# Kernel tuning notes

Hardware: AMD Instinct MI355X
Metric: run time of the kernel (lower is better)

Reference implementation:

```python
import jax, jax.numpy as jnp
import numpy as np

B, S, D, H = 4, 2048, 512, 8
HD = D // H  # head_dim = 64


def setup_inputs() -> dict:
    key = jax.random.key(0)
    ks = jax.random.split(key, 16)
    sd = 1.0 / np.sqrt(D)
    def lin(ka, kb):
        W = jax.random.uniform(ka, (D, D), jnp.float32, -sd, sd)
        b = jax.random.uniform(kb, (D,), jnp.float32, -sd, sd)
        return W, b
    Wq, bq = lin(ks[0], ks[1])
    Wk, bk = lin(ks[2], ks[3])
    Wv, bv = lin(ks[4], ks[5])
    Wo, bo = lin(ks[6], ks[7])
    Ws, bs = lin(ks[8], ks[9])
    Wsh, bsh = lin(ks[10], ks[11])
    mod1_feat = jax.random.normal(ks[12], (B, S, D), jnp.float32)
    mod2_feat = jax.random.normal(ks[13], (B, S, D), jnp.float32)
    return {"mod1_feat": mod1_feat, "mod2_feat": mod2_feat,
            "Wq": Wq, "bq": bq, "Wk": Wk, "bk": bk, "Wv": Wv, "bv": bv,
            "Wo": Wo, "bo": bo, "Ws": Ws, "bs": bs, "Wsh": Wsh, "bsh": bsh}


def _heads(x):
    # [B, S, D] -> [B, H, S, HD]
    b, s, _ = x.shape
    return x.reshape(b, s, H, HD).transpose(0, 2, 1, 3)


def reference(mod1_feat, mod2_feat, Wq, bq, Wk, bk, Wv, bv, Wo, bo, Ws, bs, Wsh, bsh):
    Q = _heads(mod1_feat @ Wq + bq)
    K = _heads(mod2_feat @ Wk + bk)
    V = _heads(mod2_feat @ Wv + bv)
    scale = _heads(mod2_feat @ Ws + bs)
    shift = _heads(mod2_feat @ Wsh + bsh)
    K = K * scale + shift
    V = V * scale + shift
    scores = jnp.einsum('bhqd,bhkd->bhqk', Q, K) / jnp.sqrt(jnp.float32(HD))
    attn = jax.nn.softmax(scores, axis=-1)
    out = jnp.einsum('bhqk,bhkd->bhqd', attn, V)  # [B, H, S, HD]
    out = out.transpose(0, 2, 1, 3).reshape(mod1_feat.shape[0], -1, H * HD)
    return out @ Wo + bo
```

## Files before the change

### kernel.cpp

```cpp
#include <hip/hip_runtime.h>
#include <hip/hip_bf16.h>
#include <cstdint>
#include <cstddef>

typedef __bf16 bf16_t;
typedef __bf16 bf16x8 __attribute__((ext_vector_type(8)));
typedef __bf16 bf16x4 __attribute__((ext_vector_type(4)));
typedef float f32x4 __attribute__((ext_vector_type(4)));

#define DEVINL static __device__ __forceinline__

constexpr int B_ = 4, S_ = 2048, D_ = 512, H_ = 8, HD_ = 64;
constexpr int M_ = B_ * S_;
constexpr int NIN = 14;

DEVINL bf16x8 load8g(const bf16_t* p) { return *reinterpret_cast<const bf16x8*>(p); }

DEVINL int swcol(int col, int row) {
  return (col & ~63) | ((((col >> 3) ^ row) & 7) << 3) | (col & 7);
}

DEVINL int pK(int row) { return (row & 3) | (((row >> 3) & 1) << 2); }
DEVINL int swcolK(int col, int row) {
  return (col & ~63) | ((((col >> 3) ^ pK(row)) & 7) << 3) | (col & 7);
}

DEVINL void gl2lds(const bf16_t* g, bf16_t* l) {
  __builtin_amdgcn_global_load_lds(
      (const __attribute__((address_space(1))) void*)g,
      (__attribute__((address_space(3))) void*)l, 16, 0, 0);
}

DEVINL void stage16(bf16_t* dst, const void* src, size_t off, bool f32) {
  if (f32) {
    const float* p = (const float*)src + off;
    bf16x8 v0, v1;
#pragma unroll
    for (int j = 0; j < 8; ++j) { v0[j] = (bf16_t)p[j]; v1[j] = (bf16_t)p[8 + j]; }
    *reinterpret_cast<bf16x8*>(dst)     = v0;
    *reinterpret_cast<bf16x8*>(dst + 8) = v1;
  } else {
    const bf16_t* p = (const bf16_t*)src + off;
    *reinterpret_cast<bf16x8*>(dst)     = load8g(p);
    *reinterpret_cast<bf16x8*>(dst + 8) = load8g(p + 8);
  }
}

DEVINL float readf(const void* p, size_t i, bool f32) {
  return f32 ? ((const float*)p)[i] : (float)((const bf16_t*)p)[i];
}

struct DetectArgs { const uint16_t* p[NIN]; int n[NIN]; int* flags; };

__global__ __launch_bounds__(64) void detect_kernel(DetectArgs a) {
  const int z = blockIdx.x;
  const uint16_t* p = a.p[z];
  const int n = a.n[z];
  const int t = threadIdx.x;
  int cnt = 0;
  for (int i = t; i < n; i += 64) {
    const int e = (p[i] >> 7) & 0xFF;
    cnt += (e >= 200);
  }
#pragma unroll
  for (int off = 32; off > 0; off >>= 1) cnt += __shfl_down(cnt, off, 64);
  if (t == 0) a.flags[z] = (cnt > 16) ? 1 : 0;
}

struct PrepArgs {
  const void* csrc[2]; bf16_t* cdst[2]; int cidx[2];
  const void* wsrc[6]; int wIdx[6]; bf16_t* wdst[6];
  const int* flags;
};

__global__ __launch_bounds__(256) void prep_kernel(PrepArgs a) {
  __shared__ bf16_t tile[64][80];
  const int bid = blockIdx.x;
  if (bid < 4096) {
    const int z = bid >> 11;
    const int bx = bid & 2047;
    const bool f32 = a.flags[a.cidx[z]] != 0;
    const size_t i = ((size_t)bx * 256 + threadIdx.x) * 8;
    const int row = (int)(i >> 9);
    const int col = (int)(i & 511);
    bf16_t* dst = a.cdst[z] + (size_t)row * 512 + swcol(col, row);
    if (f32) {
      const float* p = (const float*)a.csrc[z] + i;
      bf16x8 v;
#pragma unroll
      for (int j = 0; j < 8; ++j) v[j] = (bf16_t)p[j];
      *reinterpret_cast<bf16x8*>(dst) = v;
    } else {
      *reinterpret_cast<bf16x8*>(dst) = load8g((const bf16_t*)a.csrc[z] + i);
    }
  } else {
    const int rem = bid - 4096;
    const int w = rem >> 6;
    const int r6 = rem & 63;
    const int k0 = (r6 & 7) * 64, n0 = (r6 >> 3) * 64;
    const void* src = a.wsrc[w];
    const bool f32 = a.flags[a.wIdx[w]] != 0;
    bf16_t* dst = a.wdst[w];
    const int t = threadIdx.x;
    const int r = t >> 2, c0 = (t & 3) * 16;
    stage16(&tile[r][c0], src, (size_t)(k0 + r) * 512 + n0 + c0, f32);
    __syncthreads();
    const int orow = n0 + r;
    bf16_t* o = dst + (size_t)orow * 512;
#pragma unroll
    for (int half = 0; half < 2; ++half) {
      bf16x8 ov;
#pragma unroll
      for (int j = 0; j < 8; ++j) ov[j] = tile[c0 + half * 8 + j][r];
      *reinterpret_cast<bf16x8*>(o + swcol(k0 + c0 + half * 8, orow)) = ov;
    }
  }
}

struct GemmBatch {
  const bf16_t* A[3];
  const bf16_t* Bt[3];
  const void* bias[3]; int bIdx[3];
  void* C[3];          int cIdx[3];
  const int* flags;
};

__global__ __launch_bounds__(512) void gemm_bt_kernel(GemmBatch args) {
  constexpr int K = 512, N = 512;
  __shared__ bf16_t As[3][128][64];
  __shared__ bf16_t Bs[3][64][64];
  const int z = blockIdx.z;
  const bf16_t* Ag  = args.A[z];
  const bf16_t* Btg = args.Bt[z];
  const int m0 = blockIdx.x * 128, n0 = blockIdx.y * 64;
  const int t = threadIdx.x, lane = t & 63, wave = t >> 6;
  const int l16 = lane & 15, quad = lane >> 4;
  const int wm = wave * 16;
  const int lr = lane >> 3, lc = (lane & 7) * 8;

  auto stage = [&](int slot, int k0) {
#pragma unroll
    for (int s = 0; s < 2; ++s) {
      const int r = wm + s * 8;
      gl2lds(Ag + (size_t)(m0 + r + lr) * K + k0 + lc, &As[slot][r][0]);
    }
    gl2lds(Btg + (size_t)(n0 + wave * 8 + lr) * K + k0 + lc, &Bs[slot][wave * 8][0]);
  };

  f32x4 acc[4] = {};

  stage(0, 0);
  stage(1, 64);

  constexpr int NT = K / 64;
  int cur = 0;
  for (int kt = 0; kt < NT - 1; ++kt) {
    asm volatile("s_waitcnt vmcnt(3)\n\ts_barrier" ::: "memory");
    __builtin_amdgcn_sched_barrier(0);
    if (kt + 2 < NT) {
      const int slot2 = cur == 0 ? 2 : cur - 1;
      stage(slot2, (kt + 2) * 64);
    }
#pragma unroll
    for (int ks = 0; ks < 2; ++ks) {
      const int sw = swcol(ks * 32 + quad * 8, l16);
      bf16x8 af = *reinterpret_cast<const bf16x8*>(&As[cur][wm + l16][sw]);
      bf16x8 bfr[4];
#pragma unroll
      for (int j = 0; j < 4; ++j)
        bfr[j] = *reinterpret_cast<const bf16x8*>(&Bs[cur][j * 16 + l16][sw]);
#pragma unroll
      for (int j = 0; j < 4; ++j)
        acc[j] = __builtin_amdgcn_mfma_f32_16x16x32_bf16(af, bfr[j], acc[j], 0, 0, 0);
    }
    cur = (cur == 2) ? 0 : cur + 1;
  }
  asm volatile("s_waitcnt vmcnt(0)\n\ts_barrier" ::: "memory");
  __builtin_amdgcn_sched_barrier(0);
#pragma unroll
  for (int ks = 0; ks < 2; ++ks) {
    const int sw = swcol(ks * 32 + quad * 8, l16);
    bf16x8 af = *reinterpret_cast<const bf16x8*>(&As[cur][wm + l16][sw]);
    bf16x8 bfr[4];
#pragma unroll
    for (int j = 0; j < 4; ++j)
      bfr[j] = *reinterpret_cast<const bf16x8*>(&Bs[cur][j * 16 + l16][sw]);
#pragma unroll
    for (int j = 0; j < 4; ++j)
      acc[j] = __builtin_amdgcn_mfma_f32_16x16x32_bf16(af, bfr[j], acc[j], 0, 0, 0);
  }

  const void* biag = args.bias[z];
  void* Cg         = args.C[z];
  const bool bf32 = args.bIdx[z] >= 0 && args.flags[args.bIdx[z]];
  const bool cf32 = args.cIdx[z] >= 0 && args.flags[args.cIdx[z]];
#pragma unroll
  for (int j = 0; j < 4; ++j) {
    const int col = n0 + j * 16 + l16;
    const float bv = readf(biag, col, bf32);
    const int rowb = m0 + wm + quad * 4;
#pragma unroll
    for (int r = 0; r < 4; ++r) {
      const size_t idx = (size_t)(rowb + r) * N + col;
      const float v = acc[j][r] + bv;
      if (cf32) ((float*)Cg)[idx] = v;
      else      ((bf16_t*)Cg)[idx] = (bf16_t)v;
    }
  }
}

struct KsvArgs {
  const bf16_t* A;
  const bf16_t* Bt[4];
  const void* bias[4]; int bIdx[4];
  bf16_t* Kmod;
  bf16_t* VtT;
  const int* flags;
};

__global__ __launch_bounds__(1024) void ksv_kernel(KsvArgs args) {
  constexpr int K = 512;
  __shared__ bf16_t As[3][128][64];
  __shared__ bf16_t Bs[3][4][64][64];
  const int m0 = blockIdx.x * 128, n0 = blockIdx.y * 64;
  const int t = threadIdx.x, lane = t & 63, wave = t >> 6;
  const int l16 = lane & 15, quad = lane >> 4;
  const int wm = (wave >> 2) * 32;
  const int wn = (wave & 3) * 16;
  const int lr = lane >> 3, lc = (lane & 7) * 8;

  auto stage = [&](int slot, int k0) {
    gl2lds(args.A + (size_t)(m0 + wave * 8 + lr) * K + k0 + lc, &As[slot][wave * 8][0]);
    const int mat = wave >> 2;
    const int rb = (wave & 3) * 16;
#pragma unroll
    for (int s = 0; s < 2; ++s) {
      const int r = rb + s * 8;
      gl2lds(args.Bt[mat] + (size_t)(n0 + r + lr) * K + k0 + lc, &Bs[slot][mat][r][0]);
    }
  };

  f32x4 acc[4][2] = {};

  stage(0, 0);
  stage(1, 64);

  constexpr int NT = K / 64;
  int cur = 0;
  for (int kt = 0; kt < NT - 1; ++kt) {
    asm volatile("s_waitcnt vmcnt(3)\n\ts_barrier" ::: "memory");
    __builtin_amdgcn_sched_barrier(0);
    if (kt + 2 < NT) {
      const int slot2 = cur == 0 ? 2 : cur - 1;
      stage(slot2, (kt + 2) * 64);
    }
#pragma unroll
    for (int ks = 0; ks < 2; ++ks) {
      const int sw = swcol(ks * 32 + quad * 8, l16);
      bf16x8 af[2], bfr[4];
#pragma unroll
      for (int mi = 0; mi < 2; ++mi)
        af[mi] = *reinterpret_cast<const bf16x8*>(&As[cur][wm + mi * 16 + l16][sw]);
#pragma unroll
      for (int mat = 0; mat < 4; ++mat)
        bfr[mat] = *reinterpret_cast<const bf16x8*>(&Bs[cur][mat][wn + l16][sw]);
#pragma unroll
      for (int mat = 0; mat < 4; ++mat)
#pragma unroll
        for (int mi = 0; mi < 2; ++mi)
          acc[mat][mi] = __builtin_amdgcn_mfma_f32_16x16x32_bf16(af[mi], bfr[mat], acc[mat][mi], 0, 0, 0);
    }
    cur = (cur == 2) ? 0 : cur + 1;
  }
  asm volatile("s_waitcnt vmcnt(0)\n\ts_barrier" ::: "memory");
  __builtin_amdgcn_sched_barrier(0);
#pragma unroll
  for (int ks = 0; ks < 2; ++ks) {
    const int sw = swcol(ks * 32 + quad * 8, l16);
    bf16x8 af[2], bfr[4];
#pragma unroll
    for (int mi = 0; mi < 2; ++mi)
      af[mi] = *reinterpret_cast<const bf16x8*>(&As[cur][wm + mi * 16 + l16][sw]);
#pragma unroll
    for (int mat = 0; mat < 4; ++mat)
      bfr[mat] = *reinterpret_cast<const bf16x8*>(&Bs[cur][mat][wn + l16][sw]);
#pragma unroll
    for (int mat = 0; mat < 4; ++mat)
#pragma unroll
      for (int mi = 0; mi < 2; ++mi)
        acc[mat][mi] = __builtin_amdgcn_mfma_f32_16x16x32_bf16(af[mi], bfr[mat], acc[mat][mi], 0, 0, 0);
  }

  const int col = n0 + wn + l16;
  const float bk  = readf(args.bias[0], col, args.bIdx[0] >= 0 && args.flags[args.bIdx[0]]);
  const float bv  = readf(args.bias[1], col, args.bIdx[1] >= 0 && args.flags[args.bIdx[1]]);
  const float bs  = readf(args.bias[2], col, args.bIdx[2] >= 0 && args.flags[args.bIdx[2]]);
  const float bsh = readf(args.bias[3], col, args.bIdx[3] >= 0 && args.flags[args.bIdx[3]]);
  const int hh = col >> 6, dd = col & 63;
#pragma unroll
  for (int mi = 0; mi < 2; ++mi) {
    const int rowb = m0 + wm + mi * 16 + quad * 4;
    bf16x4 vpack;
#pragma unroll
    for (int r = 0; r < 4; ++r) {
      const int row = rowb + r;
      const float s  = acc[2][mi][r] + bs;
      const float sh = acc[3][mi][r] + bsh;
      const float kk = fmaf(acc[0][mi][r] + bk, s, sh);
      const float vv = fmaf(acc[1][mi][r] + bv, s, sh);
      args.Kmod[(size_t)row * 512 + swcolK(col, row)] = (bf16_t)kk;
      vpack[r] = (bf16_t)vv;
    }
    const int bb = rowb >> 11;
    const int ss = rowb & 2047;
    *reinterpret_cast<bf16x4*>(
        args.VtT + (((size_t)(bb * H_ + hh)) * HD_ + dd) * S_ + swcol(ss, dd)) = vpack;
  }
}

__global__ __launch_bounds__(512) void attn_kernel(const bf16_t* Q, const bf16_t* Kb,
                                                   const bf16_t* Vt, bf16_t* O) {
  __shared__ bf16_t Ks[3][64][64];
  __shared__ bf16_t Vs[3][64][64];
  const int i = blockIdx.x;
  const int xcd = i & 7, g = i >> 3;
  const int slice = xcd * 4 + (g & 3);
  const int qt = g >> 2;
  const int b = slice >> 3, h = slice & 7;
  const int t = threadIdx.x, wave = t >> 6, lane = t & 63;
  const int l16 = lane & 15, quad = lane >> 4;
  const int q0 = qt * 128 + wave * 16;
  const int lr = lane >> 3, lc = (lane & 7) * 8;

  bf16x8 ones;
#pragma unroll
  for (int j = 0; j < 8; ++j) ones[j] = (bf16_t)1.0f;

  bf16x8 qf[2];
  {
    const size_t qrow = ((size_t)b * S_ + q0 + l16) * D_ + h * HD_;
    qf[0] = load8g(Q + qrow + quad * 8);
    qf[1] = load8g(Q + qrow + 32 + quad * 8);
  }

  f32x4 oacc[4] = {};
  f32x4 lacc = {};

  const size_t kbase = (size_t)b * S_ * D_ + h * HD_;
  const size_t vbase = ((size_t)(b * H_ + h)) * HD_ * S_;

  const int rbase = ((l16 >> 2) << 3) | (l16 & 3);
  int koff[2][4];
#pragma unroll
  for (int j = 0; j < 4; ++j) {
    const int rho = rbase + (j >> 1) * 32 + (j & 1) * 4;
#pragma unroll
    for (int dc = 0; dc < 2; ++dc)
      koff[dc][j] = rho * 64 + swcolK(dc * 32 + quad * 8, rho);
  }
  const int voff[2] = { swcol(quad * 8, l16), swcol(32 + quad * 8, l16) };

  auto stage = [&](int slot, int k0) {
    const int r = wave * 8;
    gl2lds(Kb + kbase + (size_t)(k0 + r + lr) * D_ + lc, &Ks[slot][r][0]);
    gl2lds(Vt + vbase + (size_t)(r + lr) * S_ + k0 + lc, &Vs[slot][r][0]);
  };

  constexpr float CE = 0.18033688011112042f;

  auto compute = [&](int cur) {
    f32x4 sacc[4] = {};
    const bf16_t* ksbase = &Ks[cur][0][0];
#pragma unroll
    for (int dc = 0; dc < 2; ++dc) {
      bf16x8 kf[4];
#pragma unroll
      for (int j = 0; j < 4; ++j)
        kf[j] = *reinterpret_cast<const bf16x8*>(ksbase + koff[dc][j]);
#pragma unroll
      for (int j = 0; j < 4; ++j)
        sacc[j] = __builtin_amdgcn_mfma_f32_16x16x32_bf16(kf[j], qf[dc], sacc[j], 0, 0, 0);
    }
#pragma unroll
    for (int kc = 0; kc < 2; ++kc) {
      bf16x8 vf[4];
#pragma unroll
      for (int dj = 0; dj < 4; ++dj)
        vf[dj] = *reinterpret_cast<const bf16x8*>(&Vs[cur][dj * 16 + l16][voff[kc]]);
      bf16x8 bp;
#pragma unroll
      for (int r = 0; r < 4; ++r) {
        bp[r]     = (bf16_t)__builtin_amdgcn_exp2f(fminf(sacc[kc * 2][r]     * CE, 57.5f));
        bp[4 + r] = (bf16_t)__builtin_amdgcn_exp2f(fminf(sacc[kc * 2 + 1][r] * CE, 57.5f));
      }
#pragma unroll
      for (int dj = 0; dj < 4; ++dj)
        oacc[dj] = __builtin_amdgcn_mfma_f32_16x16x32_bf16(vf[dj], bp, oacc[dj], 0, 0, 0);
      lacc = __builtin_amdgcn_mfma_f32_16x16x32_bf16(ones, bp, lacc, 0, 0, 0);
    }
  };

  asm volatile("s_waitcnt vmcnt(0)" ::: "memory");
  stage(0, 0);
  stage(1, 64);

  constexpr int NT = S_ / 64;
  int cur = 0;
  for (int kt = 0; kt < NT - 1; ++kt) {
    asm volatile("s_waitcnt vmcnt(2)\n\ts_barrier" ::: "memory");
    __builtin_amdgcn_sched_barrier(0);
    if (kt + 2 < NT) {
      const int slot2 = cur == 0 ? 2 : cur - 1;
      stage(slot2, (kt + 2) * 64);
    }
    compute(cur);
    cur = (cur == 2) ? 0 : cur + 1;
  }
  asm volatile("s_waitcnt vmcnt(0)\n\ts_barrier" ::: "memory");
  __builtin_amdgcn_sched_barrier(0);
  compute(cur);

  {
    const float linv = 1.0f / fmaxf(lacc[0], 1e-30f);
    const int q = q0 + l16;
    const size_t orow = ((size_t)b * S_ + q) * D_ + h * HD_;
#pragma unroll
    for (int dj = 0; dj < 4; ++dj) {
      bf16x4 pack;
#pragma unroll
      for (int r = 0; r < 4; ++r) pack[r] = (bf16_t)(oacc[dj][r] * linv);
      *reinterpret_cast<bf16x4*>(&O[orow + swcol(dj * 16 + quad * 4, q)]) = pack;
    }
  }
}

extern "C" void kernel_launch(void* const* d_in, const int* in_sizes, int n_in,
                              void* d_out, int out_size, void* d_ws, size_t ws_size,
                              hipStream_t stream) {
  (void)n_in; (void)out_size; (void)ws_size;

  char* ws = (char*)d_ws;
  auto alloc = [&](size_t bytes) -> char* {
    char* p = ws; ws += (bytes + 255) & ~(size_t)255; return p;
  };
  int* flags = (int*)alloc(64 * sizeof(int));
  const size_t wbytes = (size_t)512 * 512 * sizeof(bf16_t);
  const size_t fbytes = (size_t)M_ * D_ * sizeof(bf16_t);
  bf16_t* wt    = (bf16_t*)alloc(6 * wbytes);
  bf16_t* m1b   = (bf16_t*)alloc(fbytes);
  bf16_t* m2b   = (bf16_t*)alloc(fbytes);
  bf16_t* q_buf = (bf16_t*)alloc(fbytes);
  bf16_t* atmp  = (bf16_t*)alloc(fbytes);
  bf16_t* kmod  = (bf16_t*)alloc(fbytes);
  bf16_t* vtb    = m1b;
  bf16_t* attn_b = atmp;

  bf16_t* wtq  = wt + 0 * 512 * 512;
  bf16_t* wtk  = wt + 1 * 512 * 512;
  bf16_t* wtv  = wt + 2 * 512 * 512;
  bf16_t* wts  = wt + 3 * 512 * 512;
  bf16_t* wtsh = wt + 4 * 512 * 512;
  bf16_t* wto  = wt + 5 * 512 * 512;

  DetectArgs da;
  for (int i = 0; i < NIN; ++i) {
    da.p[i] = (const uint16_t*)d_in[i];
    da.n[i] = in_sizes[i] < 2048 ? in_sizes[i] : 2048;
  }
  da.flags = flags;
  hipLaunchKernelGGL(detect_kernel, dim3(NIN), dim3(64), 0, stream, da);

  PrepArgs pa;
  pa.csrc[0] = d_in[0]; pa.cdst[0] = m1b; pa.cidx[0] = 0;
  pa.csrc[1] = d_in[1]; pa.cdst[1] = m2b; pa.cidx[1] = 1;
  const int widx[6] = {2, 4, 6, 10, 12, 8};
  bf16_t* wdst[6] = {wtq, wtk, wtv, wts, wtsh, wto};
  for (int i = 0; i < 6; ++i) { pa.wsrc[i] = d_in[widx[i]]; pa.wIdx[i] = widx[i]; pa.wdst[i] = wdst[i]; }
  pa.flags = flags;
  hipLaunchKernelGGL(prep_kernel, dim3(4096 + 384), dim3(256), 0, stream, pa);

  GemmBatch g1;
  g1.A[0] = m1b;  g1.A[1] = m1b;  g1.A[2] = m1b;
  g1.Bt[0] = wtq; g1.Bt[1] = wtq; g1.Bt[2] = wtq;
  g1.bias[0] = d_in[3];  g1.bIdx[0] = 3;
  g1.bias[1] = d_in[3];  g1.bIdx[1] = 3;
  g1.bias[2] = d_in[3];  g1.bIdx[2] = 3;
  g1.C[0] = q_buf; g1.cIdx[0] = -1;
  g1.C[1] = q_buf; g1.cIdx[1] = -1;
  g1.C[2] = q_buf; g1.cIdx[2] = -1;
  g1.flags = flags;
  hipLaunchKernelGGL(gemm_bt_kernel, dim3(M_ / 128, 8, 1), dim3(512), 0, stream, g1);

  KsvArgs kv;
  kv.A = m2b;
  kv.Bt[0] = wtk; kv.Bt[1] = wtv; kv.Bt[2] = wts; kv.Bt[3] = wtsh;
  kv.bias[0] = d_in[5];  kv.bIdx[0] = 5;
  kv.bias[1] = d_in[7];  kv.bIdx[1] = 7;
  kv.bias[2] = d_in[11]; kv.bIdx[2] = 11;
  kv.bias[3] = d_in[13]; kv.bIdx[3] = 13;
  kv.Kmod = kmod; kv.VtT = vtb;
  kv.flags = flags;
  hipLaunchKernelGGL(ksv_kernel, dim3(M_ / 128, 8), dim3(1024), 0, stream, kv);

  hipLaunchKernelGGL(attn_kernel, dim3(512), dim3(512), 0, stream,
                     q_buf, kmod, vtb, attn_b);

  GemmBatch g2;
  for (int i = 0; i < 3; ++i) {
    g2.A[i] = attn_b;
    g2.Bt[i] = wto;
    g2.bias[i] = d_in[9]; g2.bIdx[i] = 9;
    g2.C[i] = d_out; g2.cIdx[i] = 0;
  }
  g2.flags = flags;
  hipLaunchKernelGGL(gemm_bt_kernel, dim3(M_ / 128, 8, 1), dim3(512), 0, stream, g2);
}
```

Measured before the change: 194.8 us.

## Fuse Q projection GEMM into attention kernel prologue

Removes the separate Q projection GEMM launch. Each attention block now computes its 128x64 Q tile from mod1 and the transposed Wq slice with a triple-buffered LDS pipeline before the attention loop, and adds the bias in registers. This saves a kernel launch and the Q buffer write and re-read. The cost is extra LDS (a third buffer) and a serial prologue inside each attention block. V^T also gets its own buffer, since m1b can no longer be reused as scratch.

```diff
diff --git a/kernel.cpp b/kernel.cpp
--- a/kernel.cpp
+++ b/kernel.cpp
@@ -318,10 +318,13 @@
   }
 }
 
-__global__ __launch_bounds__(512) void attn_kernel(const bf16_t* Q, const bf16_t* Kb,
-                                                   const bf16_t* Vt, bf16_t* O) {
+__global__ __launch_bounds__(512) void attn_kernel(const bf16_t* M1, const bf16_t* Wq,
+                                                   const void* bq, const int* flags,
+                                                   const bf16_t* Kb, const bf16_t* Vt,
+                                                   bf16_t* O) {
   __shared__ bf16_t Ks[3][64][64];
   __shared__ bf16_t Vs[3][64][64];
+  __shared__ bf16_t Xs[3][64][64];
   const int i = blockIdx.x;
   const int xcd = i & 7, g = i >> 3;
   const int slice = xcd * 4 + (g & 3);
@@ -332,16 +335,79 @@
   const int q0 = qt * 128 + wave * 16;
   const int lr = lane >> 3, lc = (lane & 7) * 8;
 
+  const size_t q0g = (size_t)b * S_ + qt * 128;
+
+  auto qstage = [&](int set, int k0) {
+#pragma unroll
+    for (int s = 0; s < 2; ++s) {
+      const int r = wave * 16 + s * 8;
+      bf16_t* dst = (wave < 4) ? &Ks[set][r][0] : &Vs[set][r - 64][0];
+      gl2lds(M1 + (q0g + r + lr) * D_ + k0 + lc, dst);
+    }
+    gl2lds(Wq + (size_t)(h * HD_ + wave * 8 + lr) * D_ + k0 + lc, &Xs[set][wave * 8][0]);
+  };
+
+  f32x4 qacc[4] = {};
+  const bf16_t* brow = (wave < 4) ? &Ks[0][wave * 16][0] : &Vs[0][wave * 16 - 64][0];
+  const int setstride = 64 * 64;
+
+  auto qcompute = [&](int set) {
+    const bf16_t* bbase = brow + set * setstride;
+#pragma unroll
+    for (int ks = 0; ks < 2; ++ks) {
+      const int sw = swcol(ks * 32 + quad * 8, l16);
+      bf16x8 bf = *reinterpret_cast<const bf16x8*>(bbase + l16 * 64 + sw);
+      bf16x8 af[4];
+#pragma unroll
+      for (int j = 0; j < 4; ++j)
+        af[j] = *reinterpret_cast<const bf16x8*>(&Xs[set][j * 16 + l16][sw]);
+#pragma unroll
+      for (int j = 0; j < 4; ++j)
+        qacc[j] = __builtin_amdgcn_mfma_f32_16x16x32_bf16(af[j], bf, qacc[j], 0, 0, 0);
+    }
+  };
+
+  qstage(0, 0);
+  qstage(1, 64);
+  {
+    constexpr int QNT = D_ / 64;
+    int cur = 0;
+    for (int kt = 0; kt < QNT - 1; ++kt) {
+      asm volatile("s_waitcnt vmcnt(3)\n\ts_barrier" ::: "memory");
+      __builtin_amdgcn_sched_barrier(0);
+      if (kt + 2 < QNT) {
+        const int slot2 = cur == 0 ? 2 : cur - 1;
+        qstage(slot2, (kt + 2) * 64);
+      }
+      qcompute(cur);
+      cur = (cur == 2) ? 0 : cur + 1;
+    }
+    asm volatile("s_waitcnt vmcnt(0)\n\ts_barrier" ::: "memory");
+    __builtin_amdgcn_sched_barrier(0);
+    qcompute(cur);
+  }
+  const bool qbf32 = flags[3] != 0;
+  __syncthreads();
+  bf16_t* qls = &Xs[0][0][0];
+#pragma unroll
+  for (int j = 0; j < 4; ++j) {
+    bf16x4 pk;
+#pragma unroll
+    for (int r = 0; r < 4; ++r) {
+      const int d = j * 16 + quad * 4 + r;
+      pk[r] = (bf16_t)(qacc[j][r] + readf(bq, h * HD_ + d, qbf32));
+    }
+    *reinterpret_cast<bf16x4*>(&qls[wave * 1024 + l16 * 64 + swcol(j * 16 + quad * 4, l16)]) = pk;
+  }
+  __syncthreads();
+  bf16x8 qf[2];
+#pragma unroll
+  for (int dc = 0; dc < 2; ++dc)
+    qf[dc] = *reinterpret_cast<const bf16x8*>(&qls[wave * 1024 + l16 * 64 + swcol(dc * 32 + quad * 8, l16)]);
+
   bf16x8 ones;
 #pragma unroll
   for (int j = 0; j < 8; ++j) ones[j] = (bf16_t)1.0f;
-
-  bf16x8 qf[2];
-  {
-    const size_t qrow = ((size_t)b * S_ + q0 + l16) * D_ + h * HD_;
-    qf[0] = load8g(Q + qrow + quad * 8);
-    qf[1] = load8g(Q + qrow + 32 + quad * 8);
-  }
 
   f32x4 oacc[4] = {};
   f32x4 lacc = {};
@@ -449,10 +515,9 @@
   bf16_t* wt    = (bf16_t*)alloc(6 * wbytes);
   bf16_t* m1b   = (bf16_t*)alloc(fbytes);
   bf16_t* m2b   = (bf16_t*)alloc(fbytes);
-  bf16_t* q_buf = (bf16_t*)alloc(fbytes);
+  bf16_t* vtb   = (bf16_t*)alloc(fbytes);
   bf16_t* atmp  = (bf16_t*)alloc(fbytes);
   bf16_t* kmod  = (bf16_t*)alloc(fbytes);
-  bf16_t* vtb    = m1b;
   bf16_t* attn_b = atmp;
 
   bf16_t* wtq  = wt + 0 * 512 * 512;
@@ -478,18 +543,6 @@
   for (int i = 0; i < 6; ++i) { pa.wsrc[i] = d_in[widx[i]]; pa.wIdx[i] = widx[i]; pa.wdst[i] = wdst[i]; }
   pa.flags = flags;
   hipLaunchKernelGGL(prep_kernel, dim3(4096 + 384), dim3(256), 0, stream, pa);
-
-  GemmBatch g1;
-  g1.A[0] = m1b;  g1.A[1] = m1b;  g1.A[2] = m1b;
-  g1.Bt[0] = wtq; g1.Bt[1] = wtq; g1.Bt[2] = wtq;
-  g1.bias[0] = d_in[3];  g1.bIdx[0] = 3;
-  g1.bias[1] = d_in[3];  g1.bIdx[1] = 3;
-  g1.bias[2] = d_in[3];  g1.bIdx[2] = 3;
-  g1.C[0] = q_buf; g1.cIdx[0] = -1;
-  g1.C[1] = q_buf; g1.cIdx[1] = -1;
-  g1.C[2] = q_buf; g1.cIdx[2] = -1;
-  g1.flags = flags;
-  hipLaunchKernelGGL(gemm_bt_kernel, dim3(M_ / 128, 8, 1), dim3(512), 0, stream, g1);
 
   KsvArgs kv;
   kv.A = m2b;
@@ -503,7 +556,7 @@
   hipLaunchKernelGGL(ksv_kernel, dim3(M_ / 128, 8), dim3(1024), 0, stream, kv);
 
   hipLaunchKernelGGL(attn_kernel, dim3(512), dim3(512), 0, stream,
-                     q_buf, kmod, vtb, attn_b);
+                     m1b, wtq, d_in[3], flags, kmod, vtb, attn_b);
 
   GemmBatch g2;
   for (int i = 0; i < 3; ++i) {
```

Measured after the change: 194.9 us. Within noise of the previous version (+0.1%).
